# Performance work log

Hardware: AMD Instinct MI355X
Metric: run time of the kernel (lower is better)

The kernel has to match this reference:

```python
import jax, jax.numpy as jnp
import numpy as np

B, L, C, D = 32, 4096, 64, 128
TOPK = max(1, int(L * 0.5))


def setup_inputs() -> dict:
    key = jax.random.key(0)
    ks = jax.random.split(key, 9)
    s = lambda k, sh: jax.random.normal(k, sh, dtype=jnp.float32) * 0.02
    return {
        "x": jax.random.normal(ks[0], (B, L, C), dtype=jnp.float32),
        "score_w": s(ks[1], (C,)),
        "score_b": jnp.zeros((), jnp.float32),
        "sparse_w": s(ks[2], (C, D)),
        "sparse_b": jnp.zeros((D,), jnp.float32),
        "full_w": s(ks[3], (C, D)),
        "full_b": jnp.zeros((D,), jnp.float32),
        "ln_g": jnp.ones((D,), jnp.float32),
        "ln_b": jnp.zeros((D,), jnp.float32),
    }


def _layernorm(h, g, b, eps=1e-5):
    mu = jnp.mean(h, axis=-1, keepdims=True)
    var = jnp.mean(jnp.square(h - mu), axis=-1, keepdims=True)
    return (h - mu) * jax.lax.rsqrt(var + eps) * g + b


def reference(x, score_w, score_b, sparse_w, sparse_b, full_w, full_b, ln_g, ln_b):
    # scores: (B, L)
    scores = jnp.einsum("blc,c->bl", x, score_w) + score_b
    _, idx = jax.lax.top_k(scores, TOPK)              # (B, K)
    sparse_x = jnp.take_along_axis(x, idx[:, :, None], axis=1)  # (B, K, C)
    sparse_feat = jax.nn.gelu(jnp.einsum("bkc,cd->bkd", sparse_x, sparse_w) + sparse_b, approximate=False)
    sparse_agg = jnp.mean(sparse_feat, axis=1, keepdims=True)   # (B, 1, D)
    full_feat = jnp.einsum("blc,cd->bld", x, full_w) + full_b   # (B, L, D)
    out = _layernorm(full_feat + sparse_agg, ln_g, ln_b)
    return out
```

## Files before the change

### kernel.cpp

```cpp
#include <hip/hip_runtime.h>
#include <math.h>

static constexpr int PB = 32;
static constexpr int PL = 4096;
static constexpr int PC = 64;
static constexpr int PD = 128;
static constexpr int PK = 2048;

typedef __attribute__((ext_vector_type(8))) short bf16x8;
typedef __attribute__((ext_vector_type(4))) float f32x4;

static constexpr int LSTRIDE = 72;

__device__ inline short f2bf(float f) {
  unsigned u = __float_as_uint(f);
  u += 0x7FFFu + ((u >> 16) & 1u);
  return (short)(u >> 16);
}

__device__ inline bf16x8 load_a8(const float* p) {
  float4 f0 = *(const float4*)p;
  float4 f1 = *(const float4*)(p + 4);
  bf16x8 r;
  r[0] = f2bf(f0.x); r[1] = f2bf(f0.y); r[2] = f2bf(f0.z); r[3] = f2bf(f0.w);
  r[4] = f2bf(f1.x); r[5] = f2bf(f1.y); r[6] = f2bf(f1.z); r[7] = f2bf(f1.w);
  return r;
}

__global__ __launch_bounds__(256) void scores_kernel(
    const float* __restrict__ x, const float* __restrict__ score_w,
    const float* __restrict__ score_b, float* __restrict__ scores) {
  int tid = threadIdx.x;
  int r  = tid >> 4;
  int c4 = tid & 15;
  int row = blockIdx.x * 16 + r;
  float4 xv = *(const float4*)(x + (size_t)row * PC + c4 * 4);
  float4 wv = *(const float4*)(score_w + c4 * 4);
  float v = xv.x * wv.x + xv.y * wv.y + xv.z * wv.z + xv.w * wv.w;
  #pragma unroll
  for (int off = 1; off < 16; off <<= 1) v += __shfl_xor(v, off);
  if (c4 == 0) scores[row] = v + score_b[0];
}

__global__ __launch_bounds__(256) void select_kernel(
    const float* __restrict__ scores, int* __restrict__ selidx,
    float* __restrict__ agg) {
  __shared__ unsigned hist4[4 * 256];
  __shared__ unsigned sbuf[257];
  __shared__ unsigned wsum[4];
  __shared__ unsigned sh_prefix, sh_need;

  int tid = threadIdx.x;
  int lane = tid & 63;
  int wid  = tid >> 6;
  int b = blockIdx.x;
  const float* sc = scores + (size_t)b * PL;

  unsigned k[16];
  #pragma unroll
  for (int q = 0; q < 4; ++q) {
    float4 f = *(const float4*)(sc + tid * 16 + q * 4);
    unsigned u0 = __float_as_uint(f.x), u1 = __float_as_uint(f.y);
    unsigned u2 = __float_as_uint(f.z), u3 = __float_as_uint(f.w);
    k[q * 4 + 0] = (u0 & 0x80000000u) ? ~u0 : (u0 | 0x80000000u);
    k[q * 4 + 1] = (u1 & 0x80000000u) ? ~u1 : (u1 | 0x80000000u);
    k[q * 4 + 2] = (u2 & 0x80000000u) ? ~u2 : (u2 | 0x80000000u);
    k[q * 4 + 3] = (u3 & 0x80000000u) ? ~u3 : (u3 | 0x80000000u);
  }

  if (tid == 0) { sh_prefix = 0u; sh_need = (unsigned)PK; sbuf[256] = 0u; }
  if (tid < PD) agg[(size_t)b * PD + tid] = 0.f;

  for (int r = 3; r >= 0; --r) {
    int shift = r * 8;
    #pragma unroll
    for (int w = 0; w < 4; ++w) hist4[w * 256 + tid] = 0u;
    __syncthreads();
    unsigned prefix = sh_prefix;
    unsigned need   = sh_need;
    unsigned maskAbove = (r == 3) ? 0u : (~0u << (shift + 8));
    unsigned* myhist = &hist4[wid * 256];
    #pragma unroll
    for (int j = 0; j < 16; ++j) {
      if ((k[j] & maskAbove) == prefix)
        atomicAdd(&myhist[(k[j] >> shift) & 255u], 1u);
    }
    __syncthreads();
    unsigned v = hist4[tid] + hist4[256 + tid] + hist4[512 + tid] + hist4[768 + tid];
    #pragma unroll
    for (int off = 1; off < 64; off <<= 1) {
      unsigned t = __shfl_down(v, off);
      if (lane + off < 64) v += t;
    }
    if (lane == 0) wsum[wid] = v;
    __syncthreads();
    unsigned add = 0;
    #pragma unroll
    for (int w = 0; w < 4; ++w) if (w > wid) add += wsum[w];
    sbuf[tid] = v + add;
    __syncthreads();
    if (sbuf[tid] >= need && sbuf[tid + 1] < need) {
      sh_prefix = prefix | ((unsigned)tid << shift);
      sh_need = need - sbuf[tid + 1];
    }
  }
  __syncthreads();
  unsigned T = sh_prefix;
  unsigned needEq = sh_need;

  int base = tid * 16;
  unsigned ceq = 0;
  #pragma unroll
  for (int j = 0; j < 16; ++j) ceq += (k[j] == T);

  unsigned v1 = ceq;
  #pragma unroll
  for (int off = 1; off < 64; off <<= 1) {
    unsigned t = __shfl_up(v1, off);
    if (lane >= off) v1 += t;
  }
  if (lane == 63) wsum[wid] = v1;
  __syncthreads();
  unsigned add1 = 0;
  #pragma unroll
  for (int w = 0; w < 4; ++w) if (w < wid) add1 += wsum[w];
  unsigned eqbase = v1 + add1 - ceq;
  __syncthreads();

  unsigned csel = 0, eqr = eqbase;
  #pragma unroll
  for (int j = 0; j < 16; ++j) {
    if (k[j] > T) csel++;
    else if (k[j] == T) { if (eqr < needEq) csel++; eqr++; }
  }
  unsigned v2 = csel;
  #pragma unroll
  for (int off = 1; off < 64; off <<= 1) {
    unsigned t = __shfl_up(v2, off);
    if (lane >= off) v2 += t;
  }
  if (lane == 63) wsum[wid] = v2;
  __syncthreads();
  unsigned add2 = 0;
  #pragma unroll
  for (int w = 0; w < 4; ++w) if (w < wid) add2 += wsum[w];
  unsigned pos = v2 + add2 - csel;

  eqr = eqbase;
  int* outp = selidx + (size_t)b * PK;
  #pragma unroll
  for (int j = 0; j < 16; ++j) {
    bool sel;
    if (k[j] > T) sel = true;
    else if (k[j] == T) { sel = (eqr < needEq); eqr++; }
    else sel = false;
    if (sel) outp[pos++] = base + j;
  }
}

__device__ inline void stage_wt(const float* __restrict__ w, short* WT, int tid) {
  for (int i = tid; i < (PC / 2) * PD; i += 256) {
    int d = i & (PD - 1);
    int cp = i >> 7;
    float a = w[(size_t)(2 * cp) * PD + d];
    float c = w[(size_t)(2 * cp + 1) * PD + d];
    unsigned lo = (unsigned short)f2bf(a);
    unsigned hi = (unsigned short)f2bf(c);
    ((unsigned*)WT)[d * (LSTRIDE / 2) + cp] = lo | (hi << 16);
  }
}

__global__ __launch_bounds__(256) void sparse_kernel(
    const float* __restrict__ x, const float* __restrict__ sparse_w,
    const float* __restrict__ sparse_b, const int* __restrict__ selidx,
    float* __restrict__ agg) {
  __shared__ short WT[PD * LSTRIDE];
  __shared__ float red[PD];
  int tid = threadIdx.x;
  stage_wt(sparse_w, WT, tid);
  if (tid < PD) red[tid] = 0.f;
  __syncthreads();

  int lane = tid & 63, wid = tid >> 6;
  int ln = lane & 15, quad = lane >> 4;
  int b  = blockIdx.x >> 5;
  int rb = blockIdx.x & 31;
  int j  = rb * 64 + wid * 16 + ln;
  int row = selidx[(size_t)b * PK + j];

  const float* ap = x + ((size_t)b * PL + row) * PC + quad * 8;
  bf16x8 a0 = load_a8(ap);
  bf16x8 a1 = load_a8(ap + 32);

  f32x4 acc[8];
  #pragma unroll
  for (int t = 0; t < 8; ++t) acc[t] = (f32x4){0.f, 0.f, 0.f, 0.f};

  #pragma unroll
  for (int t = 0; t < 8; ++t) {
    const short* wp = WT + (t * 16 + ln) * LSTRIDE + quad * 8;
    bf16x8 b0 = *(const bf16x8*)wp;
    bf16x8 b1 = *(const bf16x8*)(wp + 32);
    acc[t] = __builtin_amdgcn_mfma_f32_16x16x32_bf16(a0, b0, acc[t], 0, 0, 0);
    acc[t] = __builtin_amdgcn_mfma_f32_16x16x32_bf16(a1, b1, acc[t], 0, 0, 0);
  }

  #pragma unroll
  for (int t = 0; t < 8; ++t) {
    float bias = sparse_b[t * 16 + ln];
    float s = 0.f;
    #pragma unroll
    for (int i = 0; i < 4; ++i) {
      float v = acc[t][i] + bias;
      s += 0.5f * v * (1.0f + erff(v * 0.70710678118654752f));
    }
    s += __shfl_xor(s, 16);
    s += __shfl_xor(s, 32);
    if (quad == 0) atomicAdd(&red[t * 16 + ln], s);
  }
  __syncthreads();
  if (tid < PD) atomicAdd(&agg[(size_t)b * PD + tid], red[tid]);
}

__global__ __launch_bounds__(256) void full_ln_kernel(
    const float* __restrict__ x, const float* __restrict__ full_w,
    const float* __restrict__ full_b, const float* __restrict__ ln_g,
    const float* __restrict__ ln_b, const float* __restrict__ agg,
    float* __restrict__ out) {
  __shared__ short WT[PD * LSTRIDE];
  int tid = threadIdx.x;
  stage_wt(full_w, WT, tid);
  __syncthreads();

  int lane = tid & 63, wid = tid >> 6;
  int ln = lane & 15, quad = lane >> 4;
  int rowbase = blockIdx.x * 64 + wid * 16;
  int b = rowbase >> 12;

  const float invK = 1.0f / (float)PK;
  float bias[8], gg[8], bb[8];
  #pragma unroll
  for (int t = 0; t < 8; ++t) {
    int d = t * 16 + ln;
    bias[t] = full_b[d] + agg[(size_t)b * PD + d] * invK;
    gg[t] = ln_g[d];
    bb[t] = ln_b[d];
  }

  int arow = rowbase + ln;
  const float* ap = x + (size_t)arow * PC + quad * 8;
  bf16x8 a0 = load_a8(ap);
  bf16x8 a1 = load_a8(ap + 32);

  f32x4 acc[8];
  #pragma unroll
  for (int t = 0; t < 8; ++t) acc[t] = (f32x4){0.f, 0.f, 0.f, 0.f};

  #pragma unroll
  for (int t = 0; t < 8; ++t) {
    const short* wp = WT + (t * 16 + ln) * LSTRIDE + quad * 8;
    bf16x8 b0 = *(const bf16x8*)wp;
    bf16x8 b1 = *(const bf16x8*)(wp + 32);
    acc[t] = __builtin_amdgcn_mfma_f32_16x16x32_bf16(a0, b0, acc[t], 0, 0, 0);
    acc[t] = __builtin_amdgcn_mfma_f32_16x16x32_bf16(a1, b1, acc[t], 0, 0, 0);
  }

  float s[4] = {0.f, 0.f, 0.f, 0.f}, ss[4] = {0.f, 0.f, 0.f, 0.f};
  #pragma unroll
  for (int t = 0; t < 8; ++t) {
    #pragma unroll
    for (int i = 0; i < 4; ++i) {
      float h = acc[t][i] + bias[t];
      acc[t][i] = h;
      s[i] += h;
      ss[i] += h * h;
    }
  }
  #pragma unroll
  for (int i = 0; i < 4; ++i) {
    #pragma unroll
    for (int off = 1; off < 16; off <<= 1) {
      s[i]  += __shfl_xor(s[i], off);
      ss[i] += __shfl_xor(ss[i], off);
    }
  }
  float mu[4], inv[4];
  #pragma unroll
  for (int i = 0; i < 4; ++i) {
    mu[i] = s[i] * (1.0f / 128.0f);
    float var = ss[i] * (1.0f / 128.0f) - mu[i] * mu[i];
    inv[i] = rsqrtf(var + 1e-5f);
  }
  #pragma unroll
  for (int t = 0; t < 8; ++t) {
    #pragma unroll
    for (int i = 0; i < 4; ++i) {
      int r = rowbase + quad * 4 + i;
      out[(size_t)r * PD + t * 16 + ln] = (acc[t][i] - mu[i]) * inv[i] * gg[t] + bb[t];
    }
  }
}

extern "C" void kernel_launch(void* const* d_in, const int* in_sizes, int n_in,
                              void* d_out, int out_size, void* d_ws, size_t ws_size,
                              hipStream_t stream) {
  const float* x        = (const float*)d_in[0];
  const float* score_w  = (const float*)d_in[1];
  const float* score_b  = (const float*)d_in[2];
  const float* sparse_w = (const float*)d_in[3];
  const float* sparse_b = (const float*)d_in[4];
  const float* full_w   = (const float*)d_in[5];
  const float* full_b   = (const float*)d_in[6];
  const float* ln_g     = (const float*)d_in[7];
  const float* ln_b     = (const float*)d_in[8];
  float* out = (float*)d_out;

  float* scores = (float*)d_ws;
  int*   selidx = (int*)((char*)d_ws + (size_t)PB * PL * 4);
  float* agg    = (float*)((char*)d_ws + (size_t)PB * PL * 4 + (size_t)PB * PK * 4);

  scores_kernel<<<PB * PL / 16, 256, 0, stream>>>(x, score_w, score_b, scores);
  select_kernel<<<PB, 256, 0, stream>>>(scores, selidx, agg);
  sparse_kernel<<<PB * (PK / 64), 256, 0, stream>>>(x, sparse_w, sparse_b, selidx, agg);
  full_ln_kernel<<<PB * PL / 64, 256, 0, stream>>>(x, full_w, full_b, ln_g, ln_b, agg, out);
}
```

Measured before the change: 134.7 us.

## Pre-convert x and weights to bf16 once and double rows per wave

The scores kernel now also writes a bf16 copy of x and pre-swizzled bf16 weight fragments for both projections into workspace. The sparse and full kernels then read bf16 x directly and copy weights into LDS with plain vector loads instead of converting per block. Each wave also processes 32 rows instead of 16, reusing each LDS weight fragment for two MFMAs, and the grids are halved accordingly. This cuts fp32 re-reads of x and repeated weight conversion, at the cost of an extra bf16 write of x (about 16 MB) and higher register pressure.

```diff
diff --git a/kernel.cpp b/kernel.cpp
--- a/kernel.cpp
+++ b/kernel.cpp
@@ -10,7 +10,7 @@
 typedef __attribute__((ext_vector_type(8))) short bf16x8;
 typedef __attribute__((ext_vector_type(4))) float f32x4;
 
-static constexpr int LSTRIDE = 72;
+#define MFMA_BF16(A, B, C) __builtin_amdgcn_mfma_f32_16x16x32_bf16(A, B, C, 0, 0, 0)
 
 __device__ inline short f2bf(float f) {
   unsigned u = __float_as_uint(f);
@@ -18,24 +18,37 @@
   return (short)(u >> 16);
 }
 
-__device__ inline bf16x8 load_a8(const float* p) {
-  float4 f0 = *(const float4*)p;
-  float4 f1 = *(const float4*)(p + 4);
-  bf16x8 r;
-  r[0] = f2bf(f0.x); r[1] = f2bf(f0.y); r[2] = f2bf(f0.z); r[3] = f2bf(f0.w);
-  r[4] = f2bf(f1.x); r[5] = f2bf(f1.y); r[6] = f2bf(f1.z); r[7] = f2bf(f1.w);
-  return r;
-}
-
 __global__ __launch_bounds__(256) void scores_kernel(
     const float* __restrict__ x, const float* __restrict__ score_w,
-    const float* __restrict__ score_b, float* __restrict__ scores) {
+    const float* __restrict__ score_b, const float* __restrict__ sparse_w,
+    const float* __restrict__ full_w, float* __restrict__ scores,
+    short* __restrict__ xbf, unsigned* __restrict__ wtfg) {
   int tid = threadIdx.x;
+
+  if (blockIdx.x < 2) {
+    const float* w = (blockIdx.x == 0) ? sparse_w : full_w;
+    unsigned* dst = wtfg + blockIdx.x * 4096;
+    for (int i = tid; i < 4096; i += 256) {
+      int d = i & 127, cp = i >> 7, c = cp * 2;
+      float va = w[(size_t)c * PD + d];
+      float vb = w[(size_t)(c + 1) * PD + d];
+      unsigned lo = (unsigned short)f2bf(va);
+      unsigned hi = (unsigned short)f2bf(vb);
+      int t = d >> 4, dl = d & 15, h = c >> 5, cq = (c >> 3) & 3, jp = (c & 7) >> 1;
+      dst[(((t * 2 + h) * 4 + cq) * 16 + dl) * 4 + jp] = lo | (hi << 16);
+    }
+  }
+
   int r  = tid >> 4;
   int c4 = tid & 15;
   int row = blockIdx.x * 16 + r;
   float4 xv = *(const float4*)(x + (size_t)row * PC + c4 * 4);
   float4 wv = *(const float4*)(score_w + c4 * 4);
+
+  short4 xbv;
+  xbv.x = f2bf(xv.x); xbv.y = f2bf(xv.y); xbv.z = f2bf(xv.z); xbv.w = f2bf(xv.w);
+  *(short4*)(xbf + (size_t)row * PC + c4 * 4) = xbv;
+
   float v = xv.x * wv.x + xv.y * wv.y + xv.z * wv.z + xv.w * wv.w;
   #pragma unroll
   for (int off = 1; off < 16; off <<= 1) v += __shfl_xor(v, off);
@@ -158,51 +171,52 @@
   }
 }
 
-__device__ inline void stage_wt(const float* __restrict__ w, short* WT, int tid) {
-  for (int i = tid; i < (PC / 2) * PD; i += 256) {
-    int d = i & (PD - 1);
-    int cp = i >> 7;
-    float a = w[(size_t)(2 * cp) * PD + d];
-    float c = w[(size_t)(2 * cp + 1) * PD + d];
-    unsigned lo = (unsigned short)f2bf(a);
-    unsigned hi = (unsigned short)f2bf(c);
-    ((unsigned*)WT)[d * (LSTRIDE / 2) + cp] = lo | (hi << 16);
-  }
-}
-
-__global__ __launch_bounds__(256) void sparse_kernel(
-    const float* __restrict__ x, const float* __restrict__ sparse_w,
+__device__ inline void stage_wtf(const unsigned* __restrict__ g, unsigned* lds, int tid) {
+  #pragma unroll
+  for (int q = 0; q < 4; ++q) {
+    uint4 v = *(const uint4*)(g + q * 1024 + tid * 4);
+    *(uint4*)(lds + q * 1024 + tid * 4) = v;
+  }
+}
+
+__global__ __launch_bounds__(256, 3) void sparse_kernel(
+    const short* __restrict__ xbf, const unsigned* __restrict__ wtfg,
     const float* __restrict__ sparse_b, const int* __restrict__ selidx,
     float* __restrict__ agg) {
-  __shared__ short WT[PD * LSTRIDE];
+  __shared__ unsigned WTf[4096];
   __shared__ float red[PD];
   int tid = threadIdx.x;
-  stage_wt(sparse_w, WT, tid);
+  stage_wtf(wtfg, WTf, tid);
   if (tid < PD) red[tid] = 0.f;
   __syncthreads();
 
   int lane = tid & 63, wid = tid >> 6;
   int ln = lane & 15, quad = lane >> 4;
-  int b  = blockIdx.x >> 5;
-  int rb = blockIdx.x & 31;
-  int j  = rb * 64 + wid * 16 + ln;
-  int row = selidx[(size_t)b * PK + j];
-
-  const float* ap = x + ((size_t)b * PL + row) * PC + quad * 8;
-  bf16x8 a0 = load_a8(ap);
-  bf16x8 a1 = load_a8(ap + 32);
-
-  f32x4 acc[8];
-  #pragma unroll
-  for (int t = 0; t < 8; ++t) acc[t] = (f32x4){0.f, 0.f, 0.f, 0.f};
-
+  int b  = blockIdx.x >> 4;
+  int rb = blockIdx.x & 15;
+  int j0 = rb * 128 + wid * 32 + ln;
+  const int* sel = selidx + (size_t)b * PK;
+  int r0 = sel[j0], r1 = sel[j0 + 16];
+
+  const short* xb = xbf + (size_t)b * PL * PC;
+  const short* p0 = xb + (size_t)r0 * PC + quad * 8;
+  const short* p1 = xb + (size_t)r1 * PC + quad * 8;
+  bf16x8 a00 = *(const bf16x8*)p0, a01 = *(const bf16x8*)(p0 + 32);
+  bf16x8 a10 = *(const bf16x8*)p1, a11 = *(const bf16x8*)(p1 + 32);
+
+  f32x4 acc0[8], acc1[8];
+  #pragma unroll
+  for (int t = 0; t < 8; ++t) { acc0[t] = (f32x4){0.f,0.f,0.f,0.f}; acc1[t] = (f32x4){0.f,0.f,0.f,0.f}; }
+
+  const short* wb = (const short*)WTf + lane * 8;
   #pragma unroll
   for (int t = 0; t < 8; ++t) {
-    const short* wp = WT + (t * 16 + ln) * LSTRIDE + quad * 8;
-    bf16x8 b0 = *(const bf16x8*)wp;
-    bf16x8 b1 = *(const bf16x8*)(wp + 32);
-    acc[t] = __builtin_amdgcn_mfma_f32_16x16x32_bf16(a0, b0, acc[t], 0, 0, 0);
-    acc[t] = __builtin_amdgcn_mfma_f32_16x16x32_bf16(a1, b1, acc[t], 0, 0, 0);
+    bf16x8 b0 = *(const bf16x8*)(wb + (2 * t) * 512);
+    bf16x8 b1 = *(const bf16x8*)(wb + (2 * t + 1) * 512);
+    acc0[t] = MFMA_BF16(a00, b0, acc0[t]);
+    acc0[t] = MFMA_BF16(a01, b1, acc0[t]);
+    acc1[t] = MFMA_BF16(a10, b0, acc1[t]);
+    acc1[t] = MFMA_BF16(a11, b1, acc1[t]);
   }
 
   #pragma unroll
@@ -211,8 +225,10 @@
     float s = 0.f;
     #pragma unroll
     for (int i = 0; i < 4; ++i) {
-      float v = acc[t][i] + bias;
-      s += 0.5f * v * (1.0f + erff(v * 0.70710678118654752f));
+      float v0 = acc0[t][i] + bias;
+      s += 0.5f * v0 * (1.0f + erff(v0 * 0.70710678118654752f));
+      float v1 = acc1[t][i] + bias;
+      s += 0.5f * v1 * (1.0f + erff(v1 * 0.70710678118654752f));
     }
     s += __shfl_xor(s, 16);
     s += __shfl_xor(s, 32);
@@ -222,19 +238,19 @@
   if (tid < PD) atomicAdd(&agg[(size_t)b * PD + tid], red[tid]);
 }
 
-__global__ __launch_bounds__(256) void full_ln_kernel(
-    const float* __restrict__ x, const float* __restrict__ full_w,
+__global__ __launch_bounds__(256, 3) void full_ln_kernel(
+    const short* __restrict__ xbf, const unsigned* __restrict__ wtfg,
     const float* __restrict__ full_b, const float* __restrict__ ln_g,
     const float* __restrict__ ln_b, const float* __restrict__ agg,
     float* __restrict__ out) {
-  __shared__ short WT[PD * LSTRIDE];
+  __shared__ unsigned WTf[4096];
   int tid = threadIdx.x;
-  stage_wt(full_w, WT, tid);
+  stage_wtf(wtfg, WTf, tid);
   __syncthreads();
 
   int lane = tid & 63, wid = tid >> 6;
   int ln = lane & 15, quad = lane >> 4;
-  int rowbase = blockIdx.x * 64 + wid * 16;
+  int rowbase = blockIdx.x * 128 + wid * 32;
   int b = rowbase >> 12;
 
   const float invK = 1.0f / (float)PK;
@@ -247,58 +263,61 @@
     bb[t] = ln_b[d];
   }
 
-  int arow = rowbase + ln;
-  const float* ap = x + (size_t)arow * PC + quad * 8;
-  bf16x8 a0 = load_a8(ap);
-  bf16x8 a1 = load_a8(ap + 32);
-
-  f32x4 acc[8];
-  #pragma unroll
-  for (int t = 0; t < 8; ++t) acc[t] = (f32x4){0.f, 0.f, 0.f, 0.f};
-
+  const short* p0 = xbf + (size_t)(rowbase + ln) * PC + quad * 8;
+  const short* p1 = xbf + (size_t)(rowbase + 16 + ln) * PC + quad * 8;
+  bf16x8 a00 = *(const bf16x8*)p0, a01 = *(const bf16x8*)(p0 + 32);
+  bf16x8 a10 = *(const bf16x8*)p1, a11 = *(const bf16x8*)(p1 + 32);
+
+  f32x4 acc0[8], acc1[8];
+  #pragma unroll
+  for (int t = 0; t < 8; ++t) { acc0[t] = (f32x4){0.f,0.f,0.f,0.f}; acc1[t] = (f32x4){0.f,0.f,0.f,0.f}; }
+
+  const short* wb = (const short*)WTf + lane * 8;
   #pragma unroll
   for (int t = 0; t < 8; ++t) {
-    const short* wp = WT + (t * 16 + ln) * LSTRIDE + quad * 8;
-    bf16x8 b0 = *(const bf16x8*)wp;
-    bf16x8 b1 = *(const bf16x8*)(wp + 32);
-    acc[t] = __builtin_amdgcn_mfma_f32_16x16x32_bf16(a0, b0, acc[t], 0, 0, 0);
-    acc[t] = __builtin_amdgcn_mfma_f32_16x16x32_bf16(a1, b1, acc[t], 0, 0, 0);
-  }
-
-  float s[4] = {0.f, 0.f, 0.f, 0.f}, ss[4] = {0.f, 0.f, 0.f, 0.f};
-  #pragma unroll
-  for (int t = 0; t < 8; ++t) {
-    #pragma unroll
-    for (int i = 0; i < 4; ++i) {
-      float h = acc[t][i] + bias[t];
-      acc[t][i] = h;
-      s[i] += h;
-      ss[i] += h * h;
-    }
-  }
-  #pragma unroll
-  for (int i = 0; i < 4; ++i) {
-    #pragma unroll
-    for (int off = 1; off < 16; off <<= 1) {
-      s[i]  += __shfl_xor(s[i], off);
-      ss[i] += __shfl_xor(ss[i], off);
-    }
-  }
-  float mu[4], inv[4];
-  #pragma unroll
-  for (int i = 0; i < 4; ++i) {
-    mu[i] = s[i] * (1.0f / 128.0f);
-    float var = ss[i] * (1.0f / 128.0f) - mu[i] * mu[i];
-    inv[i] = rsqrtf(var + 1e-5f);
-  }
-  #pragma unroll
-  for (int t = 0; t < 8; ++t) {
-    #pragma unroll
-    for (int i = 0; i < 4; ++i) {
-      int r = rowbase + quad * 4 + i;
-      out[(size_t)r * PD + t * 16 + ln] = (acc[t][i] - mu[i]) * inv[i] * gg[t] + bb[t];
-    }
-  }
+    bf16x8 b0 = *(const bf16x8*)(wb + (2 * t) * 512);
+    bf16x8 b1 = *(const bf16x8*)(wb + (2 * t + 1) * 512);
+    acc0[t] = MFMA_BF16(a00, b0, acc0[t]);
+    acc0[t] = MFMA_BF16(a01, b1, acc0[t]);
+    acc1[t] = MFMA_BF16(a10, b0, acc1[t]);
+    acc1[t] = MFMA_BF16(a11, b1, acc1[t]);
+  }
+
+#define LN_EPILOGUE(ACC, GOFF) do {                                          \
+    float s_[4] = {0.f,0.f,0.f,0.f}, ss_[4] = {0.f,0.f,0.f,0.f};             \
+    _Pragma("unroll")                                                        \
+    for (int t = 0; t < 8; ++t) {                                            \
+      _Pragma("unroll")                                                      \
+      for (int i = 0; i < 4; ++i) {                                          \
+        float h_ = ACC[t][i] + bias[t];                                      \
+        ACC[t][i] = h_;                                                      \
+        s_[i] += h_; ss_[i] += h_ * h_;                                      \
+      }                                                                      \
+    }                                                                        \
+    _Pragma("unroll")                                                        \
+    for (int i = 0; i < 4; ++i) {                                            \
+      _Pragma("unroll")                                                      \
+      for (int off = 1; off < 16; off <<= 1) {                               \
+        s_[i]  += __shfl_xor(s_[i], off);                                    \
+        ss_[i] += __shfl_xor(ss_[i], off);                                   \
+      }                                                                      \
+    }                                                                        \
+    _Pragma("unroll")                                                        \
+    for (int i = 0; i < 4; ++i) {                                            \
+      float mu_  = s_[i] * (1.0f / 128.0f);                                  \
+      float var_ = ss_[i] * (1.0f / 128.0f) - mu_ * mu_;                     \
+      float inv_ = rsqrtf(var_ + 1e-5f);                                     \
+      int r_ = rowbase + (GOFF) + quad * 4 + i;                              \
+      float* op_ = out + (size_t)r_ * PD + ln;                               \
+      _Pragma("unroll")                                                      \
+      for (int t = 0; t < 8; ++t)                                            \
+        op_[t * 16] = (ACC[t][i] - mu_) * inv_ * gg[t] + bb[t];              \
+    }                                                                        \
+  } while (0)
+
+  LN_EPILOGUE(acc0, 0);
+  LN_EPILOGUE(acc1, 16);
+#undef LN_EPILOGUE
 }
 
 extern "C" void kernel_launch(void* const* d_in, const int* in_sizes, int n_in,
@@ -315,12 +334,17 @@
   const float* ln_b     = (const float*)d_in[8];
   float* out = (float*)d_out;
 
-  float* scores = (float*)d_ws;
-  int*   selidx = (int*)((char*)d_ws + (size_t)PB * PL * 4);
-  float* agg    = (float*)((char*)d_ws + (size_t)PB * PL * 4 + (size_t)PB * PK * 4);
-
-  scores_kernel<<<PB * PL / 16, 256, 0, stream>>>(x, score_w, score_b, scores);
+  char* ws = (char*)d_ws;
+  float*    scores = (float*)ws;
+  int*      selidx = (int*)(ws + (512 << 10));
+  float*    agg    = (float*)(ws + (768 << 10));
+  unsigned* wtfg   = (unsigned*)(ws + (784 << 10));
+  short*    xbf    = (short*)(ws + (816 << 10));
+
+  scores_kernel<<<PB * PL / 16, 256, 0, stream>>>(x, score_w, score_b, sparse_w,
+                                                  full_w, scores, xbf, wtfg);
   select_kernel<<<PB, 256, 0, stream>>>(scores, selidx, agg);
-  sparse_kernel<<<PB * (PK / 64), 256, 0, stream>>>(x, sparse_w, sparse_b, selidx, agg);
-  full_ln_kernel<<<PB * PL / 64, 256, 0, stream>>>(x, full_w, full_b, ln_g, ln_b, agg, out);
-}
+  sparse_kernel<<<PB * (PK / 128), 256, 0, stream>>>(xbf, wtfg, sparse_b, selidx, agg);
+  full_ln_kernel<<<PB * PL / 128, 256, 0, stream>>>(xbf, wtfg + 4096, full_b,
+                                                    ln_g, ln_b, agg, out);
+}
```

Result: faster. 131.8 us (-2.1%).
